# Kernel optimization log

Hardware: AMD Instinct MI355X
Metric: run time of the kernel (lower is better)

## Reference

```python
import jax, jax.numpy as jnp
import numpy as np
import math as m

# --- renderer hyperparameters (match torch __init__ defaults) ---
BOUND = 1.125
INNER_NEAR, INNER_FAR, INNER_STEPS = 0.05, 1.0, 384
OUTER_NEAR, OUTER_FAR, OUTER_STEPS = 1.0, 100.0, 192
EPS = 1e-10
FAR_DELTA = 1e10  # delta appended after the last sample


def _z_vals_log(n_rays):
    # torch.linspace(a, b - (b-a)/steps, steps) == uniform grid excluding endpoint b
    def lin(a, b, steps):
        a, b = m.log10(a), m.log10(b)
        return jnp.linspace(a, b - (b - a) / steps, steps, dtype=jnp.float32)
    z = jnp.concatenate([lin(INNER_NEAR, INNER_FAR, INNER_STEPS),
                         lin(OUTER_NEAR, OUTER_FAR, OUTER_STEPS)], axis=0)
    return jnp.broadcast_to(z[None, :], (n_rays, z.shape[0]))  # [N, S]


def _render_rays_log(sigmas, rgbs, z_vals, z_vals_log):
    # z_vals, z_vals_log arrive quantized to fp16 (as in the torch code);
    # math is done in fp32 for stability.
    z = z_vals.astype(jnp.float32)                               # [N, S]
    delta = jnp.concatenate(
        [z[:, 1:] - z[:, :-1], jnp.full_like(z[:, :1], FAR_DELTA)], axis=-1)
    alpha = 1.0 - jnp.exp(-sigmas * delta)                       # [N, S]
    # exclusive cumulative transmittance T_i = prod_{j<i} (1 - alpha_j)
    trans = jnp.cumprod(1.0 - alpha + EPS, axis=-1)
    trans = jnp.concatenate([jnp.ones_like(trans[:, :1]), trans[:, :-1]], axis=-1)
    weights = alpha * trans                                      # [N, S]
    image = jnp.einsum('ns,nsc->nc', weights, rgbs)              # [N, 3]
    invdepth = jnp.sum(weights / z, axis=-1)                     # [N]
    return image, invdepth, weights


def setup_inputs() -> dict:
    key = jax.random.key(0)
    k1, k2, k3, k4, k5 = jax.random.split(key, 5)
    N, S = 65536, INNER_STEPS + OUTER_STEPS
    return {
        'rays_o': jax.random.normal(k1, (N, 3), dtype=jnp.float32),
        'rays_d': jax.random.normal(k2, (N, 3), dtype=jnp.float32),
        'bg_color': jax.random.uniform(k3, (3,), dtype=jnp.float32),
        'sigmas': jax.random.uniform(k4, (N, S), dtype=jnp.float32),
        'rgbs': jax.random.uniform(k5, (N, S, 3), dtype=jnp.float32),
    }


def reference(rays_o, rays_d, bg_color, sigmas, rgbs):
    n_rays = rays_o.shape[0]
    z_vals_log = _z_vals_log(n_rays)                 # [N, S] fp32
    z_vals = jnp.power(10.0, z_vals_log)             # [N, S]
    # (xyzs = rays_o + z*rays_d and mipnerf360 contraction feed the abstract
    #  network self(s_xyzs, dirs); its outputs sigmas/rgbs are inputs here.)
    image, invdepth, weights = _render_rays_log(
        sigmas, rgbs,
        z_vals.astype(jnp.float16), z_vals_log.astype(jnp.float16))
    image = image + (1.0 - jnp.sum(weights, axis=-1))[..., None] * bg_color
    return image, invdepth, weights, z_vals_log
```

## Files before the change

### kernel.cpp

```cpp
#include <hip/hip_runtime.h>
#include <hip/hip_fp16.h>

#define NS 576
#define CHUNKS 9
#define RAYS_PER_BLOCK 4

__global__ __launch_bounds__(256) void nerf_render_kernel(
    const float* __restrict__ sigmas,
    const float* __restrict__ rgbs,
    const float* __restrict__ bg,
    float* __restrict__ img,
    float* __restrict__ invd,
    float* __restrict__ wout,
    float* __restrict__ zlout,
    int N)
{
    __shared__ float s_z[NS];
    __shared__ float s_delta[NS];
    __shared__ float s_invz[NS];
    __shared__ float s_zlog[NS];

    const int tid = threadIdx.x;

    for (int s = tid; s < NS; s += 256) {
        float zl;
        if (s < 384) {
            const float start = (float)(-1.3010299956639813);
            const float stop  = (float)(-1.3010299956639813 / 384.0);
            const float step  = (stop - start) / 383.0f;
            zl = start + (float)s * step;
        } else {
            const float stop = (float)(2.0 - 2.0 / 192.0);
            const float step = stop / 191.0f;
            zl = (float)(s - 384) * step;
        }
        float z = __half2float(__float2half_rn(exp10f(zl)));
        s_zlog[s] = zl;
        s_z[s]    = z;
    }
    __syncthreads();
    for (int s = tid; s < NS; s += 256) {
        float z = s_z[s];
        s_delta[s] = (s == NS - 1) ? 1e10f : (s_z[s + 1] - z);
        s_invz[s]  = 1.0f / z;
    }
    __syncthreads();

    const int wave = tid >> 6;
    const int lane = tid & 63;
    const int ray  = blockIdx.x * RAYS_PER_BLOCK + wave;
    if (ray >= N) return;

    const float* __restrict__ sig = sigmas + (size_t)ray * NS;
    const float* __restrict__ rgb = rgbs   + (size_t)ray * NS * 3;
    float* __restrict__ wrow = wout  + (size_t)ray * NS;
    float* __restrict__ zrow = zlout + (size_t)ray * NS;

    float T = 1.0f;
    float a0 = 0.f, a1 = 0.f, a2 = 0.f;
    float id = 0.f, wsum = 0.f;

    #pragma unroll
    for (int c = 0; c < CHUNKS; ++c) {
        const int s = c * 64 + lane;
        const float sigma = sig[s];
        const float delta = s_delta[s];
        const float invz  = s_invz[s];
        const float zl    = s_zlog[s];

        const float e     = expf(-sigma * delta);
        const float alpha = 1.0f - e;
        float P = e + 1e-10f;

        #pragma unroll
        for (int off = 1; off < 64; off <<= 1) {
            float v = __shfl_up(P, off);
            if (lane >= off) P *= v;
        }

        const float prev = __shfl_up(P, 1);
        const float ex   = (lane == 0) ? T : T * prev;
        const float w    = alpha * ex;

        wrow[s] = w;
        zrow[s] = zl;

        const float r0 = rgb[3 * s + 0];
        const float r1 = rgb[3 * s + 1];
        const float r2 = rgb[3 * s + 2];
        a0 = fmaf(w, r0, a0);
        a1 = fmaf(w, r1, a1);
        a2 = fmaf(w, r2, a2);
        id = fmaf(w, invz, id);
        wsum += w;

        T *= __shfl(P, 63);
    }

    #pragma unroll
    for (int off = 32; off > 0; off >>= 1) {
        a0   += __shfl_down(a0, off);
        a1   += __shfl_down(a1, off);
        a2   += __shfl_down(a2, off);
        id   += __shfl_down(id, off);
        wsum += __shfl_down(wsum, off);
    }

    if (lane == 0) {
        const float rem = 1.0f - wsum;
        img[(size_t)ray * 3 + 0] = fmaf(rem, bg[0], a0);
        img[(size_t)ray * 3 + 1] = fmaf(rem, bg[1], a1);
        img[(size_t)ray * 3 + 2] = fmaf(rem, bg[2], a2);
        invd[ray] = id;
    }
}

extern "C" void kernel_launch(void* const* d_in, const int* in_sizes, int n_in,
                              void* d_out, int out_size, void* d_ws, size_t ws_size,
                              hipStream_t stream) {
    const int N = in_sizes[0] / 3;
    const float* sigmas = (const float*)d_in[3];
    const float* rgbs   = (const float*)d_in[4];
    const float* bg     = (const float*)d_in[2];

    float* out   = (float*)d_out;
    float* img   = out;
    float* invd  = out + (size_t)3 * N;
    float* wout  = out + (size_t)4 * N;
    float* zlout = out + (size_t)4 * N + (size_t)N * NS;

    const int blocks = (N + RAYS_PER_BLOCK - 1) / RAYS_PER_BLOCK;
    nerf_render_kernel<<<blocks, 256, 0, stream>>>(sigmas, rgbs, bg, img, invd,
                                                   wout, zlout, N);
}
```

Before: 757.3 us.

## Vectorize per-ray loads/stores with float4 and per-lane serial scan

Restructures the per-ray loop so each lane handles four consecutive samples, loading sigmas and rgbs with 128-bit vector loads and scanning the four transmittances serially before a wave-wide scan, which cuts scan rounds from nine to three. Weights and z_vals_log rows are written with nontemporal vector stores, and the z_log row is stored up front from shared memory. The aim is fewer memory instructions and better coalescing on a bandwidth-bound kernel. The cost is more registers per lane and a slightly different floating-point multiplication order in the cumulative product.

```diff
diff --git a/kernel.cpp b/kernel.cpp
--- a/kernel.cpp
+++ b/kernel.cpp
@@ -2,8 +2,9 @@
 #include <hip/hip_fp16.h>
 
 #define NS 576
-#define CHUNKS 9
 #define RAYS_PER_BLOCK 4
+
+typedef float vfloat4 __attribute__((ext_vector_type(4)));
 
 __global__ __launch_bounds__(256) void nerf_render_kernel(
     const float* __restrict__ sigmas,
@@ -15,10 +16,10 @@
     float* __restrict__ zlout,
     int N)
 {
-    __shared__ float s_z[NS];
-    __shared__ float s_delta[NS];
-    __shared__ float s_invz[NS];
-    __shared__ float s_zlog[NS];
+    __shared__ __align__(16) float s_z[NS];
+    __shared__ __align__(16) float s_delta[NS];
+    __shared__ __align__(16) float s_invz[NS];
+    __shared__ __align__(16) float s_zlog[NS];
 
     const int tid = threadIdx.x;
 
@@ -56,34 +57,92 @@
     float* __restrict__ wrow = wout  + (size_t)ray * NS;
     float* __restrict__ zrow = zlout + (size_t)ray * NS;
 
+    {
+        const vfloat4* zl4 = reinterpret_cast<const vfloat4*>(s_zlog);
+        vfloat4* zr4 = reinterpret_cast<vfloat4*>(zrow);
+        #pragma unroll
+        for (int i = 0; i < 3; ++i) {
+            const int idx = lane + 64 * i;
+            if (idx < NS / 4)
+                __builtin_nontemporal_store(zl4[idx], zr4 + idx);
+        }
+    }
+
     float T = 1.0f;
     float a0 = 0.f, a1 = 0.f, a2 = 0.f;
     float id = 0.f, wsum = 0.f;
 
     #pragma unroll
-    for (int c = 0; c < CHUNKS; ++c) {
-        const int s = c * 64 + lane;
+    for (int c = 0; c < 2; ++c) {
+        const int s0 = c * 256 + lane * 4;
+
+        const vfloat4 sg = *reinterpret_cast<const vfloat4*>(sig + s0);
+        const vfloat4 rA = *reinterpret_cast<const vfloat4*>(rgb + 3 * s0);
+        const vfloat4 rB = *reinterpret_cast<const vfloat4*>(rgb + 3 * s0 + 4);
+        const vfloat4 rC = *reinterpret_cast<const vfloat4*>(rgb + 3 * s0 + 8);
+        const vfloat4 dv = *reinterpret_cast<const vfloat4*>(&s_delta[s0]);
+        const vfloat4 iv = *reinterpret_cast<const vfloat4*>(&s_invz[s0]);
+
+        const float e0 = expf(-sg.x * dv.x);
+        const float e1 = expf(-sg.y * dv.y);
+        const float e2 = expf(-sg.z * dv.z);
+        const float e3 = expf(-sg.w * dv.w);
+        const float P0 = e0 + 1e-10f;
+        const float P1 = e1 + 1e-10f;
+        const float P2 = e2 + 1e-10f;
+        const float P3 = e3 + 1e-10f;
+
+        float sc = ((P0 * P1) * P2) * P3;
+        #pragma unroll
+        for (int off = 1; off < 64; off <<= 1) {
+            float v = __shfl_up(sc, off);
+            if (lane >= off) sc *= v;
+        }
+        const float prev = __shfl_up(sc, 1);
+        const float ex = (lane == 0) ? T : T * prev;
+
+        const float al0 = 1.0f - e0;
+        const float al1 = 1.0f - e1;
+        const float al2 = 1.0f - e2;
+        const float al3 = 1.0f - e3;
+
+        const float w0 = al0 * ex;
+        const float t1 = ex * P0;
+        const float w1 = al1 * t1;
+        const float t2 = t1 * P1;
+        const float w2 = al2 * t2;
+        const float t3 = t2 * P2;
+        const float w3 = al3 * t3;
+
+        vfloat4 wv; wv.x = w0; wv.y = w1; wv.z = w2; wv.w = w3;
+        __builtin_nontemporal_store(wv, reinterpret_cast<vfloat4*>(wrow + s0));
+
+        a0 = fmaf(w0, rA.x, a0); a0 = fmaf(w1, rA.w, a0); a0 = fmaf(w2, rB.z, a0); a0 = fmaf(w3, rC.y, a0);
+        a1 = fmaf(w0, rA.y, a1); a1 = fmaf(w1, rB.x, a1); a1 = fmaf(w2, rB.w, a1); a1 = fmaf(w3, rC.z, a1);
+        a2 = fmaf(w0, rA.z, a2); a2 = fmaf(w1, rB.y, a2); a2 = fmaf(w2, rC.x, a2); a2 = fmaf(w3, rC.w, a2);
+        id = fmaf(w0, iv.x, id); id = fmaf(w1, iv.y, id); id = fmaf(w2, iv.z, id); id = fmaf(w3, iv.w, id);
+        wsum += (w0 + w1) + (w2 + w3);
+
+        T *= __shfl(sc, 63);
+    }
+
+    {
+        const int s = 512 + lane;
         const float sigma = sig[s];
         const float delta = s_delta[s];
-        const float invz  = s_invz[s];
-        const float zl    = s_zlog[s];
-
         const float e     = expf(-sigma * delta);
         const float alpha = 1.0f - e;
         float P = e + 1e-10f;
-
         #pragma unroll
         for (int off = 1; off < 64; off <<= 1) {
             float v = __shfl_up(P, off);
             if (lane >= off) P *= v;
         }
-
         const float prev = __shfl_up(P, 1);
         const float ex   = (lane == 0) ? T : T * prev;
         const float w    = alpha * ex;
 
-        wrow[s] = w;
-        zrow[s] = zl;
+        __builtin_nontemporal_store(w, wrow + s);
 
         const float r0 = rgb[3 * s + 0];
         const float r1 = rgb[3 * s + 1];
@@ -91,10 +150,8 @@
         a0 = fmaf(w, r0, a0);
         a1 = fmaf(w, r1, a1);
         a2 = fmaf(w, r2, a2);
-        id = fmaf(w, invz, id);
+        id = fmaf(w, s_invz[s], id);
         wsum += w;
-
-        T *= __shfl(P, 63);
     }
 
     #pragma unroll
```

Result: no change. 761.8 us (+0.6%).
